# Kernel optimization log

Measured on AMD Instinct MI355X. Metric: run time of the kernel, lower is better.

Reference implementation:

```python
import jax, jax.numpy as jnp
import numpy as np

N = 100000
IN_C = 256
OUT_C = 64
E = 3200000


def _gcn_conv(x, src, dst, W, b, n_nodes):
    # Linear transform first (PyG GCNConv does lin then propagate)
    h = x @ W  # [N, out]
    # Symmetric normalization with self-loops already included in src/dst
    ones = jnp.ones(src.shape[0], dtype=h.dtype)
    deg = jax.ops.segment_sum(ones, dst, num_segments=n_nodes)  # in-degree incl self-loop
    dinv = jnp.where(deg > 0, jax.lax.rsqrt(deg), 0.0)
    norm = dinv[src] * dinv[dst]  # [E+N]
    msg = h[src] * norm[:, None]  # gather + scale
    out = jax.ops.segment_sum(msg, dst, num_segments=n_nodes)  # scatter-add
    return out + b


def setup_inputs() -> dict:
    key = jax.random.key(0)
    k1, k2, k3, k4, k5, k6 = jax.random.split(key, 6)
    x = jax.random.normal(k1, (N, IN_C), dtype=jnp.float32)
    edge_index = jax.random.randint(k2, (2, E), 0, N, dtype=jnp.int64)
    s = 1.0 / np.sqrt(IN_C)
    W_mu = jax.random.uniform(k3, (IN_C, OUT_C), jnp.float32, -s, s)
    b_mu = jnp.zeros((OUT_C,), jnp.float32)
    W_ls = jax.random.uniform(k4, (IN_C, OUT_C), jnp.float32, -s, s)
    b_ls = jnp.zeros((OUT_C,), jnp.float32)
    return {"x": x, "edge_index": edge_index, "W_mu": W_mu, "b_mu": b_mu, "W_ls": W_ls, "b_ls": b_ls}


def reference(x, edge_index, W_mu, b_mu, W_ls, b_ls):
    n_nodes = x.shape[0]
    loops = jnp.arange(n_nodes, dtype=edge_index.dtype)
    src = jnp.concatenate([edge_index[0], loops])  # add self-loops
    dst = jnp.concatenate([edge_index[1], loops])
    mu = _gcn_conv(x, src, dst, W_mu, b_mu, n_nodes)
    logstd = _gcn_conv(x, src, dst, W_ls, b_ls, n_nodes)
    return (mu, logstd)
```

## Files before the change

kernel.cpp:

```cpp
#include <hip/hip_runtime.h>
#include <hip/hip_bf16.h>


#define IN_C 256
#define HC   128
#define OC   64

__global__ void k_detect(const void* ei, int n_scan, long long nn, int* flag) {
    __shared__ int bad;
    if (threadIdx.x == 0) bad = 0;
    __syncthreads();
    const long long* p = (const long long*)ei;
    for (int i = threadIdx.x; i < n_scan; i += blockDim.x) {
        long long v = p[i];
        if (v < 0 || v >= nn) bad = 1;
    }
    __syncthreads();
    if (threadIdx.x == 0) *flag = bad;
}

__global__ __launch_bounds__(256) void k_zero(int* cnt, int* cursor, int n) {
    int i = blockIdx.x * 256 + threadIdx.x;
    if (i < n) { cnt[i] = 0; cursor[i] = 0; }
}

__global__ __launch_bounds__(256) void k_count(const void* ei, int* cnt, int E, const int* flag) {
    int e = blockIdx.x * 256 + threadIdx.x;
    if (e >= E) return;
    int d;
    if (*flag) d = ((const int*)ei)[(size_t)E + e];
    else       d = (int)((const long long*)ei)[(size_t)E + e];
    atomicAdd(&cnt[d], 1);
}

__global__ void k_scan(const int* __restrict__ cnt, int* __restrict__ rowptr, int n) {
    __shared__ int part[1024];
    const int tid = threadIdx.x;
    const int per = (n + 1023) >> 10;
    const int lo  = tid * per;
    const int hi  = min(lo + per, n);
    int s = 0;
    for (int i = lo; i < hi; ++i) s += cnt[i];
    part[tid] = s;
    __syncthreads();
    for (int off = 1; off < 1024; off <<= 1) {
        int v = (tid >= off) ? part[tid - off] : 0;
        __syncthreads();
        part[tid] += v;
        __syncthreads();
    }
    int run = (tid > 0) ? part[tid - 1] : 0;
    for (int i = lo; i < hi; ++i) { rowptr[i] = run; run += cnt[i]; }
    if (hi == n) rowptr[n] = run;
}

__global__ __launch_bounds__(256) void k_dinv(const int* __restrict__ cnt, float* dinv, int n) {
    int i = blockIdx.x * 256 + threadIdx.x;
    if (i < n) dinv[i] = rsqrtf((float)(cnt[i] + 1));
}

__global__ __launch_bounds__(256) void k_fill(const void* ei, const int* __restrict__ rowptr,
                                              int* cursor, int* __restrict__ esrc,
                                              int E, const int* flag) {
    int e = blockIdx.x * 256 + threadIdx.x;
    if (e >= E) return;
    int s, d;
    if (*flag) {
        const int* p = (const int*)ei;
        s = p[e]; d = p[(size_t)E + e];
    } else {
        const long long* p = (const long long*)ei;
        s = (int)p[e]; d = (int)p[(size_t)E + e];
    }
    int pos = rowptr[d] + atomicAdd(&cursor[d], 1);
    esrc[pos] = s;
}

#define BR 64
#define KC 32
__global__ __launch_bounds__(256) void k_gemm(const float* __restrict__ x,
                                              const float* __restrict__ Wmu,
                                              const float* __restrict__ Wls,
                                              float* __restrict__ hout, int nrows) {
    __shared__ float xs[BR][KC + 4];
    __shared__ float wsm[KC][HC];
    const int tid  = threadIdx.x;
    const int trow = tid >> 4;
    const int tcol = tid & 15;
    const int r0   = trow * 4;
    const int c0   = tcol * 4;
    const size_t rowbase = (size_t)blockIdx.x * BR;

    float acc[4][8];
    #pragma unroll
    for (int i = 0; i < 4; ++i)
        #pragma unroll
        for (int j = 0; j < 8; ++j) acc[i][j] = 0.0f;

    for (int kc = 0; kc < IN_C; kc += KC) {
        __syncthreads();
        {
            int lr = tid >> 3, lk = (tid & 7) * 4;
            #pragma unroll
            for (int half = 0; half < 2; ++half) {
                size_t gr = rowbase + lr + half * 32;
                float4 v = make_float4(0.f, 0.f, 0.f, 0.f);
                if (gr < (size_t)nrows)
                    v = *(const float4*)(x + gr * IN_C + kc + lk);
                *(float4*)&xs[lr + half * 32][lk] = v;
            }
        }
        #pragma unroll
        for (int i = 0; i < 4; ++i) {
            int q  = tid + 256 * i;
            int k  = q >> 5;
            int cq = (q & 31) * 4;
            const float* srcw = (cq < OC) ? (Wmu + (size_t)(kc + k) * OC + cq)
                                          : (Wls + (size_t)(kc + k) * OC + (cq - OC));
            *(float4*)&wsm[k][cq] = *(const float4*)srcw;
        }
        __syncthreads();

        #pragma unroll 8
        for (int k = 0; k < KC; ++k) {
            float4 w0 = *(const float4*)&wsm[k][c0];
            float4 w1 = *(const float4*)&wsm[k][c0 + OC];
            float xv[4];
            #pragma unroll
            for (int i = 0; i < 4; ++i) xv[i] = xs[r0 + i][k];
            #pragma unroll
            for (int i = 0; i < 4; ++i) {
                acc[i][0] += xv[i] * w0.x; acc[i][1] += xv[i] * w0.y;
                acc[i][2] += xv[i] * w0.z; acc[i][3] += xv[i] * w0.w;
                acc[i][4] += xv[i] * w1.x; acc[i][5] += xv[i] * w1.y;
                acc[i][6] += xv[i] * w1.z; acc[i][7] += xv[i] * w1.w;
            }
        }
    }
    #pragma unroll
    for (int i = 0; i < 4; ++i) {
        size_t gr = rowbase + r0 + i;
        if (gr < (size_t)nrows) {
            *(float4*)(hout + gr * HC + c0)      = make_float4(acc[i][0], acc[i][1], acc[i][2], acc[i][3]);
            *(float4*)(hout + gr * HC + OC + c0) = make_float4(acc[i][4], acc[i][5], acc[i][6], acc[i][7]);
        }
    }
}

__global__ __launch_bounds__(256) void k_out(const float* __restrict__ h,
                                             const int* __restrict__ rowptr,
                                             const int* __restrict__ esrc,
                                             const float* __restrict__ dinv,
                                             const float* __restrict__ bmu,
                                             const float* __restrict__ bls,
                                             float* __restrict__ out_mu,
                                             float* __restrict__ out_ls, int n) {
    int node = blockIdx.x * 4 + (threadIdx.x >> 6);
    if (node >= n) return;
    int lane = threadIdx.x & 63;
    const float2* __restrict__ h2 = (const float2*)h;

    float di = dinv[node];
    float2 self = h2[(size_t)node * 64 + lane];
    float w  = di * di;
    float ax = self.x * w, ay = self.y * w;

    int k   = rowptr[node];
    int end = rowptr[node + 1];

    for (; k + 7 < end; k += 8) {
        int   s[8];
        float nm[8];
        float2 v[8];
        #pragma unroll
        for (int u = 0; u < 8; ++u) s[u] = esrc[k + u];
        #pragma unroll
        for (int u = 0; u < 8; ++u) nm[u] = dinv[s[u]] * di;
        #pragma unroll
        for (int u = 0; u < 8; ++u) v[u] = h2[(size_t)s[u] * 64 + lane];
        #pragma unroll
        for (int u = 0; u < 8; ++u) { ax += v[u].x * nm[u]; ay += v[u].y * nm[u]; }
    }
    for (; k < end; ++k) {
        int s0 = esrc[k];
        float n0 = dinv[s0] * di;
        float2 v0 = h2[(size_t)s0 * 64 + lane];
        ax += v0.x * n0;
        ay += v0.y * n0;
    }

    if (lane < 32) {
        float2 b = ((const float2*)bmu)[lane];
        ((float2*)out_mu)[(size_t)node * 32 + lane] = make_float2(ax + b.x, ay + b.y);
    } else {
        float2 b = ((const float2*)bls)[lane - 32];
        ((float2*)out_ls)[(size_t)node * 32 + (lane - 32)] = make_float2(ax + b.x, ay + b.y);
    }
}

extern "C" void kernel_launch(void* const* d_in, const int* in_sizes, int n_in,
                              void* d_out, int out_size, void* d_ws, size_t ws_size,
                              hipStream_t stream) {
    const float* x   = (const float*)d_in[0];
    const void*  ei  = d_in[1];
    const float* Wmu = (const float*)d_in[2];
    const float* bmu = (const float*)d_in[3];
    const float* Wls = (const float*)d_in[4];
    const float* bls = (const float*)d_in[5];

    const int N = in_sizes[0] / IN_C;
    const int E = in_sizes[1] / 2;

    float* out_mu = (float*)d_out;
    float* out_ls = (float*)d_out + (size_t)N * OC;

    char* w = (char*)d_ws;
    auto align256 = [](size_t v) { return (v + 255) & ~(size_t)255; };
    int*   flag   = (int*)w;                  size_t off = 256;
    int*   cnt    = (int*)(w + off);          off += align256((size_t)N * 4);
    int*   cursor = (int*)(w + off);          off += align256((size_t)N * 4);
    float* dinv   = (float*)(w + off);        off += align256((size_t)N * 4);
    int*   rowptr = (int*)(w + off);          off += align256((size_t)(N + 1) * 4);
    int*   esrc   = (int*)(w + off);          off += align256((size_t)E * 4);
    float* h      = (float*)(w + off);        off += align256((size_t)N * HC * 4);

    int n_scan = E < 4096 ? E : 4096;
    hipLaunchKernelGGL(k_detect, dim3(1), dim3(256), 0, stream, ei, n_scan, (long long)N, flag);

    int gN = (N + 255) / 256;
    hipLaunchKernelGGL(k_zero, dim3(gN), dim3(256), 0, stream, cnt, cursor, N);

    int gE = (E + 255) / 256;
    hipLaunchKernelGGL(k_count, dim3(gE), dim3(256), 0, stream, ei, cnt, E, flag);

    hipLaunchKernelGGL(k_scan, dim3(1), dim3(1024), 0, stream, cnt, rowptr, N);
    hipLaunchKernelGGL(k_dinv, dim3(gN), dim3(256), 0, stream, cnt, dinv, N);
    hipLaunchKernelGGL(k_fill, dim3(gE), dim3(256), 0, stream, ei, rowptr, cursor, esrc, E, flag);

    int gG = (N + BR - 1) / BR;
    hipLaunchKernelGGL(k_gemm, dim3(gG), dim3(256), 0, stream, x, Wmu, Wls, h, N);

    int gO = (N + 3) / 4;
    hipLaunchKernelGGL(k_out, dim3(gO), dim3(256), 0, stream, h, rowptr, esrc, dinv, bmu, bls, out_mu, out_ls, N);
}
```

Before: 907.6 us.

## Vectorize edge loads in count/fill and enlarge GEMM register tile

The count and fill kernels now handle four edges per thread using vector loads of the edge index, which cuts the thread count and load instructions while keeping the scattered atomics. The GEMM moves to 128-row tiles with an 8x8 per-thread register block and a transposed x tile in shared memory, so the inner loop reads operands as float4 for more FMAs per shared-memory load. The transposed scalar stores into shared memory may cause bank conflicts, and the larger accumulator array raises register pressure.

```diff
diff --git a/kernel.cpp b/kernel.cpp
--- a/kernel.cpp
+++ b/kernel.cpp
@@ -25,12 +25,28 @@
 }
 
 __global__ __launch_bounds__(256) void k_count(const void* ei, int* cnt, int E, const int* flag) {
-    int e = blockIdx.x * 256 + threadIdx.x;
-    if (e >= E) return;
-    int d;
-    if (*flag) d = ((const int*)ei)[(size_t)E + e];
-    else       d = (int)((const long long*)ei)[(size_t)E + e];
-    atomicAdd(&cnt[d], 1);
+    int e0 = (blockIdx.x * 256 + threadIdx.x) * 4;
+    if (e0 >= E) return;
+    if (e0 + 3 < E) {
+        int d[4];
+        if (*flag) {
+            int4 v = *(const int4*)((const int*)ei + (size_t)E + e0);
+            d[0] = v.x; d[1] = v.y; d[2] = v.z; d[3] = v.w;
+        } else {
+            const long long* p = (const long long*)ei + (size_t)E + e0;
+            longlong2 a = *(const longlong2*)p;
+            longlong2 b = *(const longlong2*)(p + 2);
+            d[0] = (int)a.x; d[1] = (int)a.y; d[2] = (int)b.x; d[3] = (int)b.y;
+        }
+        #pragma unroll
+        for (int u = 0; u < 4; ++u) atomicAdd(&cnt[d[u]], 1);
+    } else {
+        for (int e = e0; e < E; ++e) {
+            int d = (*flag) ? ((const int*)ei)[(size_t)E + e]
+                            : (int)((const long long*)ei)[(size_t)E + e];
+            atomicAdd(&cnt[d], 1);
+        }
+    }
 }
 
 __global__ void k_scan(const int* __restrict__ cnt, int* __restrict__ rowptr, int n) {
@@ -62,57 +78,87 @@
 __global__ __launch_bounds__(256) void k_fill(const void* ei, const int* __restrict__ rowptr,
                                               int* cursor, int* __restrict__ esrc,
                                               int E, const int* flag) {
-    int e = blockIdx.x * 256 + threadIdx.x;
-    if (e >= E) return;
-    int s, d;
-    if (*flag) {
-        const int* p = (const int*)ei;
-        s = p[e]; d = p[(size_t)E + e];
+    int e0 = (blockIdx.x * 256 + threadIdx.x) * 4;
+    if (e0 >= E) return;
+    if (e0 + 3 < E) {
+        int s[4], d[4];
+        if (*flag) {
+            int4 vs = *(const int4*)((const int*)ei + e0);
+            int4 vd = *(const int4*)((const int*)ei + (size_t)E + e0);
+            s[0] = vs.x; s[1] = vs.y; s[2] = vs.z; s[3] = vs.w;
+            d[0] = vd.x; d[1] = vd.y; d[2] = vd.z; d[3] = vd.w;
+        } else {
+            const long long* ps = (const long long*)ei + e0;
+            const long long* pd = (const long long*)ei + (size_t)E + e0;
+            longlong2 a = *(const longlong2*)ps;
+            longlong2 b = *(const longlong2*)(ps + 2);
+            longlong2 c = *(const longlong2*)pd;
+            longlong2 g = *(const longlong2*)(pd + 2);
+            s[0] = (int)a.x; s[1] = (int)a.y; s[2] = (int)b.x; s[3] = (int)b.y;
+            d[0] = (int)c.x; d[1] = (int)c.y; d[2] = (int)g.x; d[3] = (int)g.y;
+        }
+        #pragma unroll
+        for (int u = 0; u < 4; ++u) {
+            int pos = rowptr[d[u]] + atomicAdd(&cursor[d[u]], 1);
+            esrc[pos] = s[u];
+        }
     } else {
-        const long long* p = (const long long*)ei;
-        s = (int)p[e]; d = (int)p[(size_t)E + e];
-    }
-    int pos = rowptr[d] + atomicAdd(&cursor[d], 1);
-    esrc[pos] = s;
-}
-
-#define BR 64
-#define KC 32
+        for (int e = e0; e < E; ++e) {
+            int s, d;
+            if (*flag) {
+                s = ((const int*)ei)[e]; d = ((const int*)ei)[(size_t)E + e];
+            } else {
+                s = (int)((const long long*)ei)[e]; d = (int)((const long long*)ei)[(size_t)E + e];
+            }
+            int pos = rowptr[d] + atomicAdd(&cursor[d], 1);
+            esrc[pos] = s;
+        }
+    }
+}
+
+#define BR2 128
+#define KC2 32
+#define STX 132
 __global__ __launch_bounds__(256) void k_gemm(const float* __restrict__ x,
                                               const float* __restrict__ Wmu,
                                               const float* __restrict__ Wls,
                                               float* __restrict__ hout, int nrows) {
-    __shared__ float xs[BR][KC + 4];
-    __shared__ float wsm[KC][HC];
+    __shared__ float xsT[KC2][STX];
+    __shared__ float wsm[KC2][STX];
     const int tid  = threadIdx.x;
     const int trow = tid >> 4;
     const int tcol = tid & 15;
-    const int r0   = trow * 4;
-    const int c0   = tcol * 4;
-    const size_t rowbase = (size_t)blockIdx.x * BR;
-
-    float acc[4][8];
+    const int r0   = trow * 8;
+    const int c0   = tcol * 8;
+    const size_t rowbase = (size_t)blockIdx.x * BR2;
+
+    float acc[8][8];
     #pragma unroll
-    for (int i = 0; i < 4; ++i)
+    for (int i = 0; i < 8; ++i)
         #pragma unroll
         for (int j = 0; j < 8; ++j) acc[i][j] = 0.0f;
 
-    for (int kc = 0; kc < IN_C; kc += KC) {
+    for (int kc = 0; kc < IN_C; kc += KC2) {
         __syncthreads();
         {
-            int lr = tid >> 3, lk = (tid & 7) * 4;
+            int kq  = tid & 7;
+            int row = tid >> 3;
             #pragma unroll
-            for (int half = 0; half < 2; ++half) {
-                size_t gr = rowbase + lr + half * 32;
+            for (int it = 0; it < 4; ++it) {
+                int r = row + it * 32;
+                size_t gr = rowbase + r;
                 float4 v = make_float4(0.f, 0.f, 0.f, 0.f);
                 if (gr < (size_t)nrows)
-                    v = *(const float4*)(x + gr * IN_C + kc + lk);
-                *(float4*)&xs[lr + half * 32][lk] = v;
+                    v = *(const float4*)(x + gr * IN_C + kc + kq * 4);
+                xsT[kq * 4 + 0][r] = v.x;
+                xsT[kq * 4 + 1][r] = v.y;
+                xsT[kq * 4 + 2][r] = v.z;
+                xsT[kq * 4 + 3][r] = v.w;
             }
         }
         #pragma unroll
-        for (int i = 0; i < 4; ++i) {
-            int q  = tid + 256 * i;
+        for (int it = 0; it < 4; ++it) {
+            int q  = tid + 256 * it;
             int k  = q >> 5;
             int cq = (q & 31) * 4;
             const float* srcw = (cq < OC) ? (Wmu + (size_t)(kc + k) * OC + cq)
@@ -121,28 +167,27 @@
         }
         __syncthreads();
 
-        #pragma unroll 8
-        for (int k = 0; k < KC; ++k) {
+        #pragma unroll
+        for (int k = 0; k < KC2; ++k) {
+            float4 a0 = *(const float4*)&xsT[k][r0];
+            float4 a1 = *(const float4*)&xsT[k][r0 + 4];
             float4 w0 = *(const float4*)&wsm[k][c0];
-            float4 w1 = *(const float4*)&wsm[k][c0 + OC];
-            float xv[4];
+            float4 w1 = *(const float4*)&wsm[k][c0 + 4];
+            float av[8] = {a0.x, a0.y, a0.z, a0.w, a1.x, a1.y, a1.z, a1.w};
+            float wv[8] = {w0.x, w0.y, w0.z, w0.w, w1.x, w1.y, w1.z, w1.w};
             #pragma unroll
-            for (int i = 0; i < 4; ++i) xv[i] = xs[r0 + i][k];
-            #pragma unroll
-            for (int i = 0; i < 4; ++i) {
-                acc[i][0] += xv[i] * w0.x; acc[i][1] += xv[i] * w0.y;
-                acc[i][2] += xv[i] * w0.z; acc[i][3] += xv[i] * w0.w;
-                acc[i][4] += xv[i] * w1.x; acc[i][5] += xv[i] * w1.y;
-                acc[i][6] += xv[i] * w1.z; acc[i][7] += xv[i] * w1.w;
-            }
+            for (int i = 0; i < 8; ++i)
+                #pragma unroll
+                for (int j = 0; j < 8; ++j)
+                    acc[i][j] += av[i] * wv[j];
         }
     }
     #pragma unroll
-    for (int i = 0; i < 4; ++i) {
+    for (int i = 0; i < 8; ++i) {
         size_t gr = rowbase + r0 + i;
         if (gr < (size_t)nrows) {
-            *(float4*)(hout + gr * HC + c0)      = make_float4(acc[i][0], acc[i][1], acc[i][2], acc[i][3]);
-            *(float4*)(hout + gr * HC + OC + c0) = make_float4(acc[i][4], acc[i][5], acc[i][6], acc[i][7]);
+            *(float4*)(hout + gr * HC + c0)     = make_float4(acc[i][0], acc[i][1], acc[i][2], acc[i][3]);
+            *(float4*)(hout + gr * HC + c0 + 4) = make_float4(acc[i][4], acc[i][5], acc[i][6], acc[i][7]);
         }
     }
 }
@@ -230,14 +275,14 @@
     int gN = (N + 255) / 256;
     hipLaunchKernelGGL(k_zero, dim3(gN), dim3(256), 0, stream, cnt, cursor, N);
 
-    int gE = (E + 255) / 256;
-    hipLaunchKernelGGL(k_count, dim3(gE), dim3(256), 0, stream, ei, cnt, E, flag);
+    int gE4 = (E + 1023) / 1024;
+    hipLaunchKernelGGL(k_count, dim3(gE4), dim3(256), 0, stream, ei, cnt, E, flag);
 
     hipLaunchKernelGGL(k_scan, dim3(1), dim3(1024), 0, stream, cnt, rowptr, N);
     hipLaunchKernelGGL(k_dinv, dim3(gN), dim3(256), 0, stream, cnt, dinv, N);
-    hipLaunchKernelGGL(k_fill, dim3(gE), dim3(256), 0, stream, ei, rowptr, cursor, esrc, E, flag);
-
-    int gG = (N + BR - 1) / BR;
+    hipLaunchKernelGGL(k_fill, dim3(gE4), dim3(256), 0, stream, ei, rowptr, cursor, esrc, E, flag);
+
+    int gG = (N + BR2 - 1) / BR2;
     hipLaunchKernelGGL(k_gemm, dim3(gG), dim3(256), 0, stream, x, Wmu, Wls, h, N);
 
     int gO = (N + 3) / 4;
```

After: 1.020 ms. 1.12x slower.
